# Optimization experiments

Hardware: AMD Instinct MI355X
Metric: run time of the kernel (lower is better)

The kernel has to match this reference:

```python
import jax, jax.numpy as jnp
import numpy as np

N, R = 100000, 200          # num_entities, num_relations
INIT, GC1, D = 100, 150, 200  # init_emb_size, gc1_emb_size, embedding_dim
C, K, B, NA, E, NC = 200, 5, 128, 8, 500000, 16
EPS = 1e-5


def _lrelu(x):
    return jnp.where(x >= 0, x, 0.01 * x)


def _bn(x, g, b):
    # eval-mode BatchNorm1d with running_mean=0, running_var=1
    return x * (g / jnp.sqrt(jnp.asarray(1.0 + EPS, x.dtype))) + b


def _gcn(x, W, bias, alpha, edge_index, edge_rel):
    # A = coo(edge_index, alpha[edge_rel]); out = (A + A^T) @ (x @ W) + bias
    alp = alpha[edge_rel, 0]              # [E]
    support = x @ W                       # [N, F]
    row, col = edge_index[0], edge_index[1]
    w = alp[:, None]
    out = jnp.zeros_like(support)
    out = out.at[row].add(w * support[col])
    out = out.at[col].add(w * support[row])
    return out + bias


def setup_inputs():
    key = jax.random.key(0)
    ks = iter(jax.random.split(key, 40))
    rn = lambda sh: 0.05 * jax.random.normal(next(ks), sh, dtype=jnp.float32)
    inp = {}
    inp["e1"] = jax.random.randint(next(ks), (B, 1), 0, N)
    inp["rel"] = jax.random.randint(next(ks), (B, 1), 0, R)
    inp["attr"] = jax.random.randint(next(ks), (B, 1, NA), 0, N)
    inp["X"] = jnp.arange(N)
    inp["edge_index"] = jax.random.randint(next(ks), (2, E), 0, N)
    inp["edge_rel"] = jax.random.randint(next(ks), (E,), 0, R)
    inp["emb_e"] = rn((N, INIT))
    inp["emb_rel"] = rn((R, D))
    inp["alpha1"] = rn((R + 1, 1))
    inp["alpha2"] = rn((R + 1, 1))
    inp["gc1_W"] = rn((INIT, GC1)); inp["gc1_b"] = rn((GC1,))
    inp["gc2_W"] = rn((GC1, D)); inp["gc2_b"] = rn((D,))
    inp["bn3_g"] = jnp.ones(GC1); inp["bn3_b"] = jnp.zeros(GC1)
    inp["bn4_g"] = jnp.ones(D); inp["bn4_b"] = jnp.zeros(D)
    inp["bn0_g"] = jnp.ones(2); inp["bn0_b"] = jnp.zeros(2)
    inp["conv_w"] = rn((C, 2, K)); inp["conv_b"] = rn((C,))
    inp["bn1_g"] = jnp.ones(C); inp["bn1_b"] = jnp.zeros(C)
    inp["fc_w"] = rn((D, C * D)); inp["fc_b"] = rn((D,))
    inp["bn2_g"] = jnp.ones(D); inp["bn2_b"] = jnp.zeros(D)
    inp["bi_w"] = rn((D, D)); inp["bi_b"] = rn((D,))
    inp["si_w"] = rn((D, D)); inp["si_b"] = rn((D,))
    inp["cs_w"] = rn((D, 2 * D)); inp["cs_b"] = rn((D,))
    inp["fc2_w"] = rn((NC, D)); inp["fc2_b"] = rn((NC,))
    return inp


def reference(e1, rel, attr, X, edge_index, edge_rel, emb_e, emb_rel, alpha1, alpha2,
              gc1_W, gc1_b, gc2_W, gc2_b, bn3_g, bn3_b, bn4_g, bn4_b, bn0_g, bn0_b,
              conv_w, conv_b, bn1_g, bn1_b, fc_w, fc_b, bn2_g, bn2_b,
              bi_w, bi_b, si_w, si_b, cs_w, cs_b, fc2_w, fc2_b):
    emb_initial = emb_e[X]                                  # [N, INIT]
    x = _gcn(emb_initial, gc1_W, gc1_b, alpha1, edge_index, edge_rel)
    x = jnp.tanh(_bn(x, bn3_g, bn3_b))                      # [N, GC1]
    x = _gcn(x, gc2_W, gc2_b, alpha2, edge_index, edge_rel)
    all_emb = jnp.tanh(_bn(x, bn4_g, bn4_b))                # [N, D]

    e1_emb = all_emb[e1]                                    # [B, 1, D]
    rel_emb = emb_rel[rel]                                  # [B, 1, D]
    s = jnp.concatenate([e1_emb, rel_emb], axis=1)          # [B, 2, D]
    s = _bn(s, bn0_g[None, :, None], bn0_b[None, :, None])
    x = jax.lax.conv_general_dilated(s, conv_w, (1,), [(K // 2, K // 2)],
                                     dimension_numbers=("NCH", "OIH", "NCH"))
    x = x + conv_b[None, :, None]                           # [B, C, D]
    x = jax.nn.relu(_bn(x, bn1_g[None, :, None], bn1_b[None, :, None]))
    x = x.reshape(B, C * D) @ fc_w.T + fc_b                 # [B, D]
    x = jax.nn.relu(_bn(x, bn2_g, bn2_b))                   # user_embedding

    feats = all_emb[attr][:, 0]                             # [B, NA, D]
    ssum = feats.sum(axis=1)                                # [B, D]
    deep = 0.5 * (ssum ** 2 - (feats ** 2).sum(axis=1))     # FM interaction
    nfm = _lrelu(deep @ bi_w.T + bi_b) + _lrelu(ssum @ si_w.T + si_b)
    user = _lrelu(jnp.concatenate([nfm, x], axis=-1) @ cs_w.T + cs_b)  # [B, D]

    pred = jax.nn.sigmoid(user @ all_emb.T)                 # [B, N]
    clusters = jax.nn.sigmoid(user @ fc2_w.T + fc2_b)       # [B, NC]
    return pred, clusters
```

## Files before the change

kernel.cpp:

```cpp
#include <hip/hip_runtime.h>
#include <hip/hip_bf16.h>
#include <math.h>

#define NNODES 100000
#define INIT_F 100
#define GC1_F  150
#define D_F    200
#define CCH    200
#define BB     128
#define NA_    8
#define EDG    500000
#define NCL    16

#define MROWS  100032
#define MT_    (MROWS/64)

#define KPE    104
#define KP1    128
#define KP2    160
#define KPP    224
#define FCK    40000

#define NPB    256
#define NBUK   ((NNODES + NPB - 1)/NPB)
#define BCAP   4096

#define ALO ((long)128*KPP)
#define BLO ((long)256*KPP)

typedef __attribute__((ext_vector_type(8))) __bf16 bf16x8;
typedef __attribute__((ext_vector_type(4))) float  f32x4;

__device__ __forceinline__ float fast_tanh(float z){
  float ex = __expf(2.f*z);
  return 1.f - 2.f/(ex + 1.f);
}


__global__ __launch_bounds__(256) void bucket_a_k(
    const int* __restrict__ ei, const int* __restrict__ erel,
    int* __restrict__ bcur, int2* __restrict__ blist)
{
  __shared__ int hist[NBUK];
  int t = threadIdx.x;
  for (int i = t; i < NBUK; i += 256) hist[i] = 0;
  __syncthreads();
  int e0 = blockIdx.x*1024;
  int rr[4], cc[4], pl[4], rkA[4], rkB[4];
  #pragma unroll
  for (int i = 0; i < 4; i++){
    int e = e0 + i*256 + t;
    bool ok = e < EDG;
    rr[i] = ok ? ei[e]       : -1;
    cc[i] = ok ? ei[EDG + e] : 0;
    pl[i] = (ok ? erel[e] : 0) << 17;
    if (ok){
      rkA[i] = atomicAdd(&hist[rr[i] >> 8], 1);
      rkB[i] = atomicAdd(&hist[cc[i] >> 8], 1);
    }
  }
  __syncthreads();
  for (int i = t; i < NBUK; i += 256){
    int c = hist[i];
    hist[i] = c ? atomicAdd(&bcur[i], c) : 0;
  }
  __syncthreads();
  #pragma unroll
  for (int i = 0; i < 4; i++){
    if (rr[i] < 0) continue;
    int bA = rr[i] >> 8, bB = cc[i] >> 8;
    int sA = hist[bA] + rkA[i];
    int sB = hist[bB] + rkB[i];
    if (sA < BCAP) blist[(long)bA*BCAP + sA] = make_int2(rr[i], cc[i] | pl[i]);
    if (sB < BCAP) blist[(long)bB*BCAP + sB] = make_int2(cc[i], rr[i] | pl[i]);
  }
}

__global__ __launch_bounds__(256) void bucket_b_k(
    const int2* __restrict__ blist, const int* __restrict__ bcur,
    unsigned* __restrict__ adjW, int* __restrict__ start_, int* __restrict__ deg_)
{
  __shared__ int cnt[NPB];
  __shared__ int sc[NPB];
  int b = blockIdx.x, t = threadIdx.x;
  cnt[t] = 0;
  __syncthreads();
  int n = min(bcur[b], BCAP);
  const int2* bl = blist + (long)b*BCAP;
  for (int i = t; i < n; i += 256) atomicAdd(&cnt[bl[i].x & (NPB-1)], 1);
  __syncthreads();
  int v = cnt[t]; sc[t] = v; __syncthreads();
  for (int off = 1; off < NPB; off <<= 1){
    int x = (t >= off) ? sc[t-off] : 0;
    __syncthreads();
    sc[t] += x; __syncthreads();
  }
  int excl = sc[t] - v;
  int node = b*NPB + t;
  if (node < NNODES){ start_[node] = b*BCAP + excl; deg_[node] = v; }
  cnt[t] = excl;
  __syncthreads();
  for (int i = t; i < n; i += 256){
    int2 rec = bl[i];
    int s = atomicAdd(&cnt[rec.x & (NPB-1)], 1);
    adjW[(long)b*BCAP + s] = (unsigned)rec.y;
  }
}


template<int G, int LPG, int PIN, int POUT>
__global__ __launch_bounds__(256) void gather_g(
    const __bf16* __restrict__ X, const int* __restrict__ start,
    const int* __restrict__ degv, const unsigned* __restrict__ adjW,
    const float* __restrict__ alpha, __bf16* __restrict__ Z)
{
  int wave = threadIdx.x >> 6;
  int lane = threadIdx.x & 63;
  int v = blockIdx.x*4 + wave;
  if (v >= NNODES) return;
  int grp = lane / LPG;
  int li  = lane - grp*LPG;
  bool act = grp < G;
  int s = start[v], e = s + degv[v];
  float acc[8] = {};
  for (int jb = s; jb < e; jb += 4*G){
    int   u[4];
    float wt[4];
    #pragma unroll
    for (int q = 0; q < 4; q++){
      int j = jb + grp + q*G;
      u[q] = 0; wt[q] = 0.f;
      if (act && j < e){ unsigned pr = adjW[j]; u[q] = pr & 0x1FFFF; wt[q] = alpha[pr >> 17]; }
    }
    bf16x8 rows[4];
    #pragma unroll
    for (int q = 0; q < 4; q++)
      rows[q] = *(const bf16x8*)(X + (long)u[q]*PIN + li*8);
    #pragma unroll
    for (int q = 0; q < 4; q++)
      #pragma unroll
      for (int i = 0; i < 8; i++)
        acc[i] += wt[q]*(float)rows[q][i];
  }
  #pragma unroll
  for (int g = 1; g < G; g++){
    #pragma unroll
    for (int i = 0; i < 8; i++)
      acc[i] += __shfl(acc[i], lane + g*LPG, 64);
  }
  if (lane < LPG){
    bf16x8 o;
    #pragma unroll
    for (int i = 0; i < 8; i++) o[i] = (__bf16)acc[i];
    *(bf16x8*)(Z + (long)v*POUT + lane*8) = o;
  } else if (lane < POUT/8){
    bf16x8 o = {};
    *(bf16x8*)(Z + (long)v*POUT + lane*8) = o;
  }
}


template<int KP, int PHO, int NTILE>
__global__ __launch_bounds__(256) void mfma_gcn(
    const __bf16* __restrict__ A, const __bf16* __restrict__ Bt,
    __bf16* __restrict__ C,
    const float* __restrict__ gb, const float* __restrict__ bng,
    const float* __restrict__ bnb, int M, int N)
{
  int id = blockIdx.x;
  int x = id & 7, j = id >> 3;
  int stripe = x + 8*(j / NTILE);
  int nt = j - (j / NTILE)*NTILE;
  if (stripe >= MT_) return;
  int w = threadIdx.x >> 6, l = threadIdx.x & 63;
  int m0 = stripe*64 + w*16;
  int n0 = nt*64;
  int ml = l & 15, kq = l >> 4;
  const __bf16* Ap = A  + (long)(m0 + ml)*KP + kq*8;
  const __bf16* Bp = Bt + (long)(n0 + ml)*KP + kq*8;
  f32x4 acc[4] = {};
  #pragma unroll
  for (int k0 = 0; k0 < KP; k0 += 32){
    bf16x8 a = *(const bf16x8*)(Ap + k0);
    #pragma unroll
    for (int t = 0; t < 4; t++){
      bf16x8 b = *(const bf16x8*)(Bp + (long)t*16*KP + k0);
      acc[t] = __builtin_amdgcn_mfma_f32_16x16x32_bf16(a, b, acc[t], 0, 0, 0);
    }
  }
  const float inv = rsqrtf(1.0f + 1e-5f);
  int mr = m0 + kq*4;
  #pragma unroll
  for (int t = 0; t < 4; t++){
    int gn = n0 + t*16 + ml;
    if (gn >= PHO) continue;
    bool real = gn < N;
    float gbb = real ? gb[gn] : 0.f;
    float sc  = real ? bng[gn]*inv : 0.f;
    float bb_ = real ? bnb[gn] : 0.f;
    #pragma unroll
    for (int r = 0; r < 4; r++){
      int gm = mr + r;
      if (gm < M){
        float xg = real ? fast_tanh((acc[t][r] + gbb)*sc + bb_) : 0.f;
        C[(long)gm*PHO + gn] = (__bf16)xg;
      }
    }
  }
}


template<int KP, int ACT, int WPB>
__global__ __launch_bounds__(WPB*64) void mfma_gemm(
    const __bf16* __restrict__ A, const __bf16* __restrict__ Bt,
    float* __restrict__ C, long ldc, int M, int N)
{
  int w = threadIdx.x >> 6, l = threadIdx.x & 63;
  int m0 = blockIdx.y*(WPB*16) + w*16;
  int n0 = blockIdx.x*64;
  int ml = l & 15, kq = l >> 4;
  const __bf16* Ap = A  + (long)(m0 + ml)*KP + kq*8;
  const __bf16* Bp = Bt + (long)(n0 + ml)*KP + kq*8;
  f32x4 acc[4] = {};
  #pragma unroll
  for (int k0 = 0; k0 < KP; k0 += 32){
    bf16x8 a = *(const bf16x8*)(Ap + k0);
    #pragma unroll
    for (int t = 0; t < 4; t++){
      bf16x8 b = *(const bf16x8*)(Bp + (long)t*16*KP + k0);
      acc[t] = __builtin_amdgcn_mfma_f32_16x16x32_bf16(a, b, acc[t], 0, 0, 0);
    }
  }
  int mr = m0 + kq*4;
  #pragma unroll
  for (int t = 0; t < 4; t++){
    int gn = n0 + t*16 + ml;
    if (gn >= N) continue;
    #pragma unroll
    for (int r = 0; r < 4; r++){
      int gm = mr + r;
      if (gm < M){
        float x = acc[t][r];
        if (ACT == 2) x = 1.f/(1.f + __expf(-x));
        C[(long)gm*ldc + gn] = x;
      }
    }
  }
}


__global__ __launch_bounds__(256) void mfma_fc_k(
    const __bf16* __restrict__ A, const __bf16* __restrict__ Bt,
    float* __restrict__ C, int M, int N, int klen)
{
  int w = threadIdx.x >> 6, l = threadIdx.x & 63;
  int m0 = blockIdx.y*64 + w*16;
  int n0 = blockIdx.x*128;
  long kb = (long)blockIdx.z * klen;
  int ml = l & 15, kq = l >> 4;
  const __bf16* Ap = A  + (long)(m0 + ml)*FCK + kb + kq*8;
  const __bf16* Bp = Bt + (long)(n0 + ml)*FCK + kb + kq*8;
  f32x4 acc[2][4] = {};
  #pragma unroll 2
  for (int k0 = 0; k0 < klen; k0 += 32){
    bf16x8 a = *(const bf16x8*)(Ap + k0);
    #pragma unroll
    for (int c = 0; c < 2; c++)
      #pragma unroll
      for (int t = 0; t < 4; t++){
        bf16x8 b = *(const bf16x8*)(Bp + (long)(c*64 + t*16)*FCK + k0);
        acc[c][t] = __builtin_amdgcn_mfma_f32_16x16x32_bf16(a, b, acc[c][t], 0, 0, 0);
      }
  }
  int mr = m0 + kq*4;
  #pragma unroll
  for (int c = 0; c < 2; c++)
    #pragma unroll
    for (int t = 0; t < 4; t++){
      int gn = n0 + c*64 + t*16 + ml;
      if (gn >= N) continue;
      #pragma unroll
      for (int r = 0; r < 4; r++){
        int gm = mr + r;
        if (gm < M) atomicAdd(&C[(long)gm*N + gn], acc[c][t][r]);
      }
    }
}


template<int NPROD, int COMBINE, bool SPLITOUT>
__global__ __launch_bounds__(256) void mfma_head_k(
    const __bf16* __restrict__ A0, const __bf16* __restrict__ B0,
    const __bf16* __restrict__ A1, const __bf16* __restrict__ B1,
    const float* __restrict__ bias0, const float* __restrict__ bias1,
    float* __restrict__ outF, __bf16* __restrict__ outS,
    int ldc, int N)
{
  int w = threadIdx.x >> 6, l = threadIdx.x & 63;
  int m0 = blockIdx.y*64 + w*16;
  int n0 = blockIdx.x*64;
  int ml = l & 15, kq = l >> 4;
  long aoff = (long)(m0 + ml)*KPP + kq*8;
  long boff = (long)(n0 + ml)*KPP + kq*8;
  f32x4 accA[4] = {}, accB[4] = {};
  #pragma unroll
  for (int k0 = 0; k0 < KPP; k0 += 32){
    bf16x8 ah = *(const bf16x8*)(A0 + aoff + k0);
    bf16x8 al = *(const bf16x8*)(A0 + ALO + aoff + k0);
    #pragma unroll
    for (int t = 0; t < 4; t++){
      bf16x8 bh = *(const bf16x8*)(B0 + boff + (long)t*16*KPP + k0);
      bf16x8 bl = *(const bf16x8*)(B0 + BLO + boff + (long)t*16*KPP + k0);
      accA[t] = __builtin_amdgcn_mfma_f32_16x16x32_bf16(ah, bh, accA[t], 0, 0, 0);
      accA[t] = __builtin_amdgcn_mfma_f32_16x16x32_bf16(al, bh, accA[t], 0, 0, 0);
      accA[t] = __builtin_amdgcn_mfma_f32_16x16x32_bf16(ah, bl, accA[t], 0, 0, 0);
    }
    if constexpr (NPROD == 2){
      bf16x8 ch = *(const bf16x8*)(A1 + aoff + k0);
      bf16x8 cl = *(const bf16x8*)(A1 + ALO + aoff + k0);
      #pragma unroll
      for (int t = 0; t < 4; t++){
        bf16x8 bh = *(const bf16x8*)(B1 + boff + (long)t*16*KPP + k0);
        bf16x8 bl = *(const bf16x8*)(B1 + BLO + boff + (long)t*16*KPP + k0);
        accB[t] = __builtin_amdgcn_mfma_f32_16x16x32_bf16(ch, bh, accB[t], 0, 0, 0);
        accB[t] = __builtin_amdgcn_mfma_f32_16x16x32_bf16(cl, bh, accB[t], 0, 0, 0);
        accB[t] = __builtin_amdgcn_mfma_f32_16x16x32_bf16(ch, bl, accB[t], 0, 0, 0);
      }
    }
  }
  int mr = m0 + kq*4;
  #pragma unroll
  for (int t = 0; t < 4; t++){
    int gn = n0 + t*16 + ml;
    if (SPLITOUT){ if (gn >= KPP) continue; }
    else         { if (gn >= N)   continue; }
    bool real = gn < N;
    float bb0 = real ? bias0[gn] : 0.f;
    float bb1 = (COMBINE == 0 && real) ? bias1[gn] : 0.f;
    #pragma unroll
    for (int r = 0; r < 4; r++){
      int gm = mr + r;
      float x;
      if (COMBINE == 0){
        float xa = accA[t][r] + bb0; xa = (xa >= 0.f) ? xa : 0.01f*xa;
        float xb = accB[t][r] + bb1; xb = (xb >= 0.f) ? xb : 0.01f*xb;
        x = xa + xb;
      } else if (COMBINE == 1){
        x = accA[t][r] + accB[t][r] + bb0;
        x = (x >= 0.f) ? x : 0.01f*x;
      } else {
        x = accA[t][r] + bb0;
        x = 1.f/(1.f + __expf(-x));
      }
      if (!real) x = 0.f;
      if (SPLITOUT){
        __bf16 h = (__bf16)x;
        outS[(long)gm*KPP + gn] = h;
        outS[ALO + (long)gm*KPP + gn] = (__bf16)(x - (float)h);
      } else {
        outF[(long)gm*ldc + gn] = x;
      }
    }
  }
}


__global__ __launch_bounds__(256) void emb_to_bf16_k(const float* __restrict__ src,
                                                     __bf16* __restrict__ dst){
  int lane = threadIdx.x & 63;
  int half = lane >> 5, l = lane & 31;
  long r = (long)blockIdx.x*8 + (threadIdx.x >> 6)*2 + half;
  if (r >= NNODES || l >= 26) return;
  float4 v = make_float4(0.f, 0.f, 0.f, 0.f);
  if (l < 25) v = *(const float4*)(src + r*INIT_F + l*4);
  __bf16 o[4] __attribute__((aligned(8))) =
      {(__bf16)v.x, (__bf16)v.y, (__bf16)v.z, (__bf16)v.w};
  *reinterpret_cast<uint2*>(dst + r*KPE + l*4) = *reinterpret_cast<const uint2*>(o);
}

__global__ void transpose_w_k(const float* __restrict__ W, __bf16* __restrict__ Bt,
                              int K, int N, int Kp){
  int n = blockIdx.x;
  for (int k = threadIdx.x; k < Kp; k += blockDim.x){
    float v = (k < K && n < N) ? W[(long)k*N + n] : 0.f;
    Bt[(long)n*Kp + k] = (__bf16)v;
  }
}

__global__ void f32_to_bf16_flat_k(const float4* __restrict__ src,
                                   __bf16* __restrict__ dst, long n4){
  long i = (long)blockIdx.x*256 + threadIdx.x;
  if (i >= n4) return;
  float4 v = src[i];
  __bf16 o[4] __attribute__((aligned(8))) =
      {(__bf16)v.x, (__bf16)v.y, (__bf16)v.z, (__bf16)v.w};
  *reinterpret_cast<uint2*>(dst + i*4) = *reinterpret_cast<const uint2*>(o);
}

__global__ void head_wsplit_k(const float* __restrict__ bi, const float* __restrict__ si,
                              const float* __restrict__ cs, const float* __restrict__ fc2,
                              __bf16* __restrict__ W){
  int k = threadIdx.x; if (k >= KPP) return;
  int n = blockIdx.x;
  int mat = blockIdx.y;
  float v = 0.f;
  if (k < D_F){
    if      (mat == 0){ if (n < D_F) v = bi[(long)n*D_F + k]; }
    else if (mat == 1){ if (n < D_F) v = si[(long)n*D_F + k]; }
    else if (mat == 2){ if (n < D_F) v = cs[(long)n*2*D_F + k]; }
    else if (mat == 3){ if (n < D_F) v = cs[(long)n*2*D_F + D_F + k]; }
    else              { if (n < NCL) v = fc2[(long)n*D_F + k]; }
  }
  __bf16 h = (__bf16)v;
  long base = (long)mat*2*BLO + (long)n*KPP + k;
  W[base]       = h;
  W[base + BLO] = (__bf16)(v - (float)h);
}


__global__ void conv_bn_relu_k(const int* __restrict__ e1, const int* __restrict__ rel,
                               const __bf16* __restrict__ AEh, const float* __restrict__ embrel,
                               const float* __restrict__ g0, const float* __restrict__ b0,
                               const float* __restrict__ cw, const float* __restrict__ cb,
                               const float* __restrict__ g1, const float* __restrict__ b1,
                               __bf16* __restrict__ out){
  __shared__ float sh[2][D_F];
  int b = blockIdx.y, c0 = blockIdx.x*8, t = threadIdx.x;
  const float inv = rsqrtf(1.0f + 1e-5f);
  if (t < D_F){
    sh[0][t] = (float)AEh[(long)e1[b]*KPP + t] * (g0[0]*inv) + b0[0];
    sh[1][t] = embrel[(long)rel[b]*D_F + t]    * (g0[1]*inv) + b0[1];
  }
  __syncthreads();
  if (t >= D_F) return;
  for (int cc = 0; cc < 8; cc++){
    int c = c0 + cc;
    float sum = cb[c];
    #pragma unroll
    for (int i = 0; i < 2; i++){
      #pragma unroll
      for (int k = 0; k < 5; k++){
        int h = t + k - 2;
        float sv = (h >= 0 && h < D_F) ? sh[i][h] : 0.f;
        sum += sv * cw[(c*2+i)*5 + k];
      }
    }
    float x = sum * (g1[c]*inv) + b1[c];
    out[((long)b*CCH + c)*D_F + t] = (__bf16)fmaxf(x, 0.f);
  }
}

__global__ void fc_fin_k(const float* __restrict__ raw, const float* __restrict__ fb,
                         const float* __restrict__ g, const float* __restrict__ bb,
                         __bf16* __restrict__ x2s){
  int b = blockIdx.x, t = threadIdx.x;
  if (t >= KPP) return;
  float x = 0.f;
  if (t < D_F){
    const float inv = rsqrtf(1.0f + 1e-5f);
    x = (raw[b*D_F + t] + fb[t]) * (g[t]*inv) + bb[t];
    x = fmaxf(x, 0.f);
  }
  __bf16 h = (__bf16)x;
  x2s[(long)b*KPP + t] = h;
  x2s[ALO + (long)b*KPP + t] = (__bf16)(x - (float)h);
}

__global__ void feats_k(const int* __restrict__ attr, const __bf16* __restrict__ AEh,
                        __bf16* __restrict__ hA){
  int b = blockIdx.x, t = threadIdx.x;
  if (t >= KPP) return;
  float s = 0.f, sq = 0.f;
  if (t < D_F){
    #pragma unroll
    for (int a = 0; a < NA_; a++){
      int id = attr[b*NA_ + a];
      float v = (float)AEh[(long)id*KPP + t];
      s += v; sq += v*v;
    }
  }
  float dp = 0.5f*(s*s - sq);
  long o = (long)b*KPP + t;
  __bf16 hd = (__bf16)dp;
  hA[o]            = hd;
  hA[o + ALO]      = (__bf16)(dp - (float)hd);
  __bf16 hs = (__bf16)s;
  hA[o + 2*ALO]    = hs;
  hA[o + 3*ALO]    = (__bf16)(s - (float)hs);
}


extern "C" void kernel_launch(void* const* d_in, const int* in_sizes, int n_in,
                              void* d_out, int out_size, void* d_ws, size_t ws_size,
                              hipStream_t stream) {
  const int* e1       = (const int*)d_in[0];
  const int* rel      = (const int*)d_in[1];
  const int* attr     = (const int*)d_in[2];
  const int* ei       = (const int*)d_in[4];
  const int* erel     = (const int*)d_in[5];
  const float* emb_e  = (const float*)d_in[6];
  const float* embrel = (const float*)d_in[7];
  const float* alpha1 = (const float*)d_in[8];
  const float* alpha2 = (const float*)d_in[9];
  const float* gc1_W  = (const float*)d_in[10];
  const float* gc1_b  = (const float*)d_in[11];
  const float* gc2_W  = (const float*)d_in[12];
  const float* gc2_b  = (const float*)d_in[13];
  const float* bn3_g  = (const float*)d_in[14];
  const float* bn3_b  = (const float*)d_in[15];
  const float* bn4_g  = (const float*)d_in[16];
  const float* bn4_b  = (const float*)d_in[17];
  const float* bn0_g  = (const float*)d_in[18];
  const float* bn0_b  = (const float*)d_in[19];
  const float* conv_w = (const float*)d_in[20];
  const float* conv_b = (const float*)d_in[21];
  const float* bn1_g  = (const float*)d_in[22];
  const float* bn1_b  = (const float*)d_in[23];
  const float* fc_w   = (const float*)d_in[24];
  const float* fc_b   = (const float*)d_in[25];
  const float* bn2_g  = (const float*)d_in[26];
  const float* bn2_b  = (const float*)d_in[27];
  const float* bi_w   = (const float*)d_in[28];
  const float* bi_b   = (const float*)d_in[29];
  const float* si_w   = (const float*)d_in[30];
  const float* si_b   = (const float*)d_in[31];
  const float* cs_w   = (const float*)d_in[32];
  const float* cs_b   = (const float*)d_in[33];
  const float* fc2_w  = (const float*)d_in[34];
  const float* fc2_b  = (const float*)d_in[35];

  float* pred_out = (float*)d_out;
  float* clus_out = (float*)d_out + (long)BB*NNODES;

  char* w = (char*)d_ws;
  size_t off = 0;
  auto alloc = [&](size_t bytes) -> void* {
    off = (off + 255) & ~(size_t)255;
    void* p = w + off;
    off += bytes;
    return p;
  };
  __bf16* AEh  = (__bf16*)alloc((size_t)MROWS*KPP*2);
  void* bufA   = alloc((size_t)MROWS*KPE*2);
  void* bufB   = alloc((size_t)MROWS*KP1*2);
  __bf16* H1h  = (__bf16*)alloc((size_t)MROWS*KP2*2);
  __bf16* Z2   = (__bf16*)alloc((size_t)MROWS*KP2*2);

  int* bcur   = (int*)alloc((size_t)NBUK*4);
  int* start_ = (int*)alloc((size_t)NNODES*4);
  int* deg    = (int*)alloc((size_t)NNODES*4);
  int2* blist = (int2*)alloc((size_t)NBUK*BCAP*8);
  unsigned* adjW = (unsigned*)alloc((size_t)NBUK*BCAP*4);
  __bf16* Bt1 = (__bf16*)alloc((size_t)192*KP1*2);
  __bf16* Bt2 = (__bf16*)alloc((size_t)256*KP2*2);
  __bf16* headW = (__bf16*)alloc((size_t)5*2*256*KPP*2);
  __bf16* headA = (__bf16*)alloc((size_t)5*2*128*KPP*2);
  float* x2raw  = (float*)alloc((size_t)BB*D_F*4);

  __bf16* emb_h   = (__bf16*)bufA;
  __bf16* fcBt    = (__bf16*)bufA;
  __bf16* Z1      = (__bf16*)bufB;
  __bf16* convout = (__bf16*)bufB;

  auto HAp = [&](int slot){ return headA + (size_t)slot*2*ALO; };
  auto HWp = [&](int mat){ return headW + (size_t)mat*2*BLO; };

  const int GGB = (NNODES + 3)/4;
  const int MT = MROWS/64;
  const int SWZB = 8*((MT + 7)/8);

  hipMemsetAsync(bcur, 0, (size_t)NBUK*4, stream);
  hipMemsetAsync(x2raw, 0, (size_t)BB*D_F*4, stream);
  bucket_a_k<<<(EDG + 1023)/1024, 256, 0, stream>>>(ei, erel, bcur, blist);
  bucket_b_k<<<NBUK, 256, 0, stream>>>(blist, bcur, adjW, start_, deg);

  emb_to_bf16_k<<<(NNODES + 7)/8, 256, 0, stream>>>(emb_e, emb_h);
  transpose_w_k<<<192, 128, 0, stream>>>(gc1_W, Bt1, INIT_F, GC1_F, KP1);
  transpose_w_k<<<256, 128, 0, stream>>>(gc2_W, Bt2, GC1_F, D_F, KP2);
  head_wsplit_k<<<dim3(256,5), 256, 0, stream>>>(bi_w, si_w, cs_w, fc2_w, headW);

  gather_g<4,13,KPE,KP1><<<GGB, 256, 0, stream>>>(emb_h, start_, deg, adjW, alpha1, Z1);
  mfma_gcn<KP1,KP2,3><<<SWZB*3, 256, 0, stream>>>(Z1, Bt1, H1h,
                                                  gc1_b, bn3_g, bn3_b, NNODES, GC1_F);

  gather_g<3,20,KP2,KP2><<<GGB, 256, 0, stream>>>(H1h, start_, deg, adjW, alpha2, Z2);
  mfma_gcn<KP2,KPP,4><<<SWZB*4, 256, 0, stream>>>(Z2, Bt2, AEh,
                                                  gc2_b, bn4_g, bn4_b, NNODES, D_F);

  {
    dim3 grid(CCH/8, BB);
    conv_bn_relu_k<<<grid, 256, 0, stream>>>(e1, rel, AEh, embrel, bn0_g, bn0_b,
                                             conv_w, conv_b, bn1_g, bn1_b, convout);
  }
  {
    long n4 = (long)D_F*FCK/4;
    f32_to_bf16_flat_k<<<(int)((n4 + 255)/256), 256, 0, stream>>>(
        (const float4*)fc_w, fcBt, n4);
  }
  {
    dim3 grid(2, 2, 125);
    mfma_fc_k<<<grid, 256, 0, stream>>>(convout, fcBt, x2raw, BB, D_F, 320);
  }
  fc_fin_k<<<BB, 256, 0, stream>>>(x2raw, fc_b, bn2_g, bn2_b, HAp(2));

  feats_k<<<BB, 256, 0, stream>>>(attr, AEh, headA);
  {
    dim3 grid(4, 2);
    mfma_head_k<2,0,true><<<grid, 256, 0, stream>>>(
        HAp(0), HWp(0), HAp(1), HWp(1), bi_b, si_b, nullptr, HAp(3), 0, D_F);
    mfma_head_k<2,1,true><<<grid, 256, 0, stream>>>(
        HAp(3), HWp(2), HAp(2), HWp(3), cs_b, nullptr, nullptr, HAp(4), 0, D_F);
  }

  {
    dim3 grid(MT, 1);
    mfma_gemm<KPP,2,8><<<grid, 512, 0, stream>>>(HAp(4), AEh, pred_out, NNODES, BB, NNODES);
  }
  {
    dim3 grid(1, 2);
    mfma_head_k<1,2,false><<<grid, 256, 0, stream>>>(
        HAp(4), HWp(4), nullptr, nullptr, fc2_b, nullptr, clus_out, nullptr, NCL, NCL);
  }
}
```

Baseline: 606.6 us.

## Fuse GCN sparse gather with MFMA projection through shared memory

Result: no change. 609.8 us (+0.5%).

```diff
diff --git a/kernel.cpp b/kernel.cpp
--- a/kernel.cpp
+++ b/kernel.cpp
@@ -108,88 +108,84 @@
 }
 
 
-template<int G, int LPG, int PIN, int POUT>
-__global__ __launch_bounds__(256) void gather_g(
+template<int G, int LPG, int PIN, int KP, int PHO>
+__global__ __launch_bounds__(1024) void gcn_layer_k(
     const __bf16* __restrict__ X, const int* __restrict__ start,
     const int* __restrict__ degv, const unsigned* __restrict__ adjW,
-    const float* __restrict__ alpha, __bf16* __restrict__ Z)
+    const float* __restrict__ alpha,
+    const __bf16* __restrict__ Bt, __bf16* __restrict__ C,
+    const float* __restrict__ gb, const float* __restrict__ bng,
+    const float* __restrict__ bnb, int M, int N)
 {
-  int wave = threadIdx.x >> 6;
+  constexpr int KPAD = KP + 8;
+  __shared__ __bf16 As[64][KPAD];
+  int w = threadIdx.x >> 6;
   int lane = threadIdx.x & 63;
-  int v = blockIdx.x*4 + wave;
-  if (v >= NNODES) return;
+  int vbase = blockIdx.x*64;
   int grp = lane / LPG;
   int li  = lane - grp*LPG;
   bool act = grp < G;
-  int s = start[v], e = s + degv[v];
-  float acc[8] = {};
-  for (int jb = s; jb < e; jb += 4*G){
-    int   u[4];
-    float wt[4];
-    #pragma unroll
-    for (int q = 0; q < 4; q++){
-      int j = jb + grp + q*G;
-      u[q] = 0; wt[q] = 0.f;
-      if (act && j < e){ unsigned pr = adjW[j]; u[q] = pr & 0x1FFFF; wt[q] = alpha[pr >> 17]; }
-    }
-    bf16x8 rows[4];
-    #pragma unroll
-    for (int q = 0; q < 4; q++)
-      rows[q] = *(const bf16x8*)(X + (long)u[q]*PIN + li*8);
-    #pragma unroll
-    for (int q = 0; q < 4; q++)
+
+  for (int q4 = 0; q4 < 4; q4++){
+    int row = w*4 + q4;
+    int v = vbase + row;
+    float acc[8] = {};
+    if (v < NNODES){
+      int s = start[v], e = s + degv[v];
+      for (int jb = s; jb < e; jb += 4*G){
+        int u[4]; float wt[4];
+        #pragma unroll
+        for (int q = 0; q < 4; q++){
+          int j = jb + grp + q*G;
+          u[q] = 0; wt[q] = 0.f;
+          if (act && j < e){ unsigned pr = adjW[j]; u[q] = pr & 0x1FFFF; wt[q] = alpha[pr >> 17]; }
+        }
+        bf16x8 rows[4];
+        #pragma unroll
+        for (int q = 0; q < 4; q++)
+          rows[q] = *(const bf16x8*)(X + (long)u[q]*PIN + li*8);
+        #pragma unroll
+        for (int q = 0; q < 4; q++)
+          #pragma unroll
+          for (int i = 0; i < 8; i++)
+            acc[i] += wt[q]*(float)rows[q][i];
+      }
       #pragma unroll
-      for (int i = 0; i < 8; i++)
-        acc[i] += wt[q]*(float)rows[q][i];
-  }
-  #pragma unroll
-  for (int g = 1; g < G; g++){
-    #pragma unroll
-    for (int i = 0; i < 8; i++)
-      acc[i] += __shfl(acc[i], lane + g*LPG, 64);
-  }
-  if (lane < LPG){
-    bf16x8 o;
-    #pragma unroll
-    for (int i = 0; i < 8; i++) o[i] = (__bf16)acc[i];
-    *(bf16x8*)(Z + (long)v*POUT + lane*8) = o;
-  } else if (lane < POUT/8){
-    bf16x8 o = {};
-    *(bf16x8*)(Z + (long)v*POUT + lane*8) = o;
-  }
-}
-
-
-template<int KP, int PHO, int NTILE>
-__global__ __launch_bounds__(256) void mfma_gcn(
-    const __bf16* __restrict__ A, const __bf16* __restrict__ Bt,
-    __bf16* __restrict__ C,
-    const float* __restrict__ gb, const float* __restrict__ bng,
-    const float* __restrict__ bnb, int M, int N)
-{
-  int id = blockIdx.x;
-  int x = id & 7, j = id >> 3;
-  int stripe = x + 8*(j / NTILE);
-  int nt = j - (j / NTILE)*NTILE;
-  if (stripe >= MT_) return;
-  int w = threadIdx.x >> 6, l = threadIdx.x & 63;
-  int m0 = stripe*64 + w*16;
-  int n0 = nt*64;
-  int ml = l & 15, kq = l >> 4;
-  const __bf16* Ap = A  + (long)(m0 + ml)*KP + kq*8;
+      for (int g = 1; g < G; g++)
+        #pragma unroll
+        for (int i = 0; i < 8; i++)
+          acc[i] += __shfl(acc[i], lane + g*LPG, 64);
+    }
+    if (lane < LPG){
+      bf16x8 o;
+      #pragma unroll
+      for (int i = 0; i < 8; i++) o[i] = (__bf16)acc[i];
+      *(bf16x8*)(&As[row][lane*8]) = o;
+    } else if (lane < KP/8){
+      bf16x8 o = {};
+      *(bf16x8*)(&As[row][lane*8]) = o;
+    }
+  }
+  __syncthreads();
+
+  int wrow = w & 3, wcol = w >> 2;
+  int n0 = wcol*64;
+  if (n0 >= PHO) return;
+  int ml = lane & 15, kq = lane >> 4;
+  int m0 = wrow*16;
   const __bf16* Bp = Bt + (long)(n0 + ml)*KP + kq*8;
-  f32x4 acc[4] = {};
+  f32x4 acc2[4] = {};
   #pragma unroll
   for (int k0 = 0; k0 < KP; k0 += 32){
-    bf16x8 a = *(const bf16x8*)(Ap + k0);
+    bf16x8 a = *(const bf16x8*)(&As[m0 + ml][kq*8 + k0]);
     #pragma unroll
     for (int t = 0; t < 4; t++){
       bf16x8 b = *(const bf16x8*)(Bp + (long)t*16*KP + k0);
-      acc[t] = __builtin_amdgcn_mfma_f32_16x16x32_bf16(a, b, acc[t], 0, 0, 0);
+      acc2[t] = __builtin_amdgcn_mfma_f32_16x16x32_bf16(a, b, acc2[t], 0, 0, 0);
     }
   }
   const float inv = rsqrtf(1.0f + 1e-5f);
-  int mr = m0 + kq*4;
+  int mr = vbase + m0 + kq*4;
   #pragma unroll
   for (int t = 0; t < 4; t++){
     int gn = n0 + t*16 + ml;
@@ -202,7 +198,7 @@
     for (int r = 0; r < 4; r++){
       int gm = mr + r;
       if (gm < M){
-        float xg = real ? fast_tanh((acc[t][r] + gbb)*sc + bb_) : 0.f;
+        float xg = real ? fast_tanh((acc2[t][r] + gbb)*sc + bb_) : 0.f;
         C[(long)gm*PHO + gn] = (__bf16)xg;
       }
     }
@@ -542,16 +538,15 @@
   };
   __bf16* AEh  = (__bf16*)alloc((size_t)MROWS*KPP*2);
   void* bufA   = alloc((size_t)MROWS*KPE*2);
-  void* bufB   = alloc((size_t)MROWS*KP1*2);
+  void* bufB   = alloc((size_t)BB*FCK*2);
   __bf16* H1h  = (__bf16*)alloc((size_t)MROWS*KP2*2);
-  __bf16* Z2   = (__bf16*)alloc((size_t)MROWS*KP2*2);
 
   int* bcur   = (int*)alloc((size_t)NBUK*4);
   int* start_ = (int*)alloc((size_t)NNODES*4);
   int* deg    = (int*)alloc((size_t)NNODES*4);
   int2* blist = (int2*)alloc((size_t)NBUK*BCAP*8);
   unsigned* adjW = (unsigned*)alloc((size_t)NBUK*BCAP*4);
-  __bf16* Bt1 = (__bf16*)alloc((size_t)192*KP1*2);
+  __bf16* Bt1 = (__bf16*)alloc((size_t)256*KP1*2);
   __bf16* Bt2 = (__bf16*)alloc((size_t)256*KP2*2);
   __bf16* headW = (__bf16*)alloc((size_t)5*2*256*KPP*2);
   __bf16* headA = (__bf16*)alloc((size_t)5*2*128*KPP*2);
@@ -559,15 +554,12 @@
 
   __bf16* emb_h   = (__bf16*)bufA;
   __bf16* fcBt    = (__bf16*)bufA;
-  __bf16* Z1      = (__bf16*)bufB;
   __bf16* convout = (__bf16*)bufB;
 
   auto HAp = [&](int slot){ return headA + (size_t)slot*2*ALO; };
   auto HWp = [&](int mat){ return headW + (size_t)mat*2*BLO; };
 
-  const int GGB = (NNODES + 3)/4;
   const int MT = MROWS/64;
-  const int SWZB = 8*((MT + 7)/8);
 
   hipMemsetAsync(bcur, 0, (size_t)NBUK*4, stream);
   hipMemsetAsync(x2raw, 0, (size_t)BB*D_F*4, stream);
@@ -575,17 +567,15 @@
   bucket_b_k<<<NBUK, 256, 0, stream>>>(blist, bcur, adjW, start_, deg);
 
   emb_to_bf16_k<<<(NNODES + 7)/8, 256, 0, stream>>>(emb_e, emb_h);
-  transpose_w_k<<<192, 128, 0, stream>>>(gc1_W, Bt1, INIT_F, GC1_F, KP1);
+  transpose_w_k<<<256, 128, 0, stream>>>(gc1_W, Bt1, INIT_F, GC1_F, KP1);
   transpose_w_k<<<256, 128, 0, stream>>>(gc2_W, Bt2, GC1_F, D_F, KP2);
   head_wsplit_k<<<dim3(256,5), 256, 0, stream>>>(bi_w, si_w, cs_w, fc2_w, headW);
 
-  gather_g<4,13,KPE,KP1><<<GGB, 256, 0, stream>>>(emb_h, start_, deg, adjW, alpha1, Z1);
-  mfma_gcn<KP1,KP2,3><<<SWZB*3, 256, 0, stream>>>(Z1, Bt1, H1h,
-                                                  gc1_b, bn3_g, bn3_b, NNODES, GC1_F);
-
-  gather_g<3,20,KP2,KP2><<<GGB, 256, 0, stream>>>(H1h, start_, deg, adjW, alpha2, Z2);
-  mfma_gcn<KP2,KPP,4><<<SWZB*4, 256, 0, stream>>>(Z2, Bt2, AEh,
-                                                  gc2_b, bn4_g, bn4_b, NNODES, D_F);
+  gcn_layer_k<4,13,KPE,KP1,KP2><<<MT, 1024, 0, stream>>>(
+      emb_h, start_, deg, adjW, alpha1, Bt1, H1h, gc1_b, bn3_g, bn3_b, NNODES, GC1_F);
+
+  gcn_layer_k<3,20,KP2,KP2,KPP><<<MT, 1024, 0, stream>>>(
+      H1h, start_, deg, adjW, alpha2, Bt2, AEh, gc2_b, bn4_g, bn4_b, NNODES, D_F);
 
   {
     dim3 grid(CCH/8, BB);
```
